# Performance work log

Measured on AMD Instinct MI355X. Metric: run time of the kernel, lower is better.

The kernel has to match this reference:

```python
import jax, jax.numpy as jnp
import numpy as np

B, N, D, H = 2, 2048, 1024, 16
HD = D // H
EPS = 1e-5

def _ln(x, g, b):
    m = jnp.mean(x, axis=-1, keepdims=True)
    v = jnp.mean((x - m) ** 2, axis=-1, keepdims=True)
    return (x - m) * jax.lax.rsqrt(v + EPS) * g + b

def setup_inputs() -> dict:
    key = jax.random.key(0)
    ks = jax.random.split(key, 16)
    s = 0.02
    inp = {
        'x': jax.random.normal(ks[0], (B, N, D), jnp.float32),
        'ln1_g': jnp.ones((D,), jnp.float32), 'ln1_b': jnp.zeros((D,), jnp.float32),
        'w_in': jax.random.normal(ks[1], (D, D), jnp.float32) * s, 'b_in': jnp.zeros((D,), jnp.float32),
        'wq': jax.random.normal(ks[2], (D, D), jnp.float32) * s,
        'wk': jax.random.normal(ks[3], (D, D), jnp.float32) * s,
        'wv': jax.random.normal(ks[4], (D, D), jnp.float32) * s,
        'wo': jax.random.normal(ks[5], (D, D), jnp.float32) * s, 'bo': jnp.zeros((D,), jnp.float32),
        'ln2_g': jnp.ones((D,), jnp.float32), 'ln2_b': jnp.zeros((D,), jnp.float32),
        'w_up': jax.random.normal(ks[6], (D, 4 * D), jnp.float32) * s, 'b_up': jnp.zeros((4 * D,), jnp.float32),
        'w_gate': jax.random.normal(ks[7], (D, 4 * D), jnp.float32) * s, 'b_gate': jnp.zeros((4 * D,), jnp.float32),
        'w_down': jax.random.normal(ks[8], (4 * D, D), jnp.float32) * s, 'b_down': jnp.zeros((D,), jnp.float32),
        'top_k': 64,
    }
    return inp

def _sparse_attention(h, wq, wk, wv, wo, bo, top_k):
    q = (h @ wq).reshape(B, N, H, HD).transpose(0, 2, 1, 3)  # [B,H,N,hd]
    k = (h @ wk).reshape(B, N, H, HD).transpose(0, 2, 1, 3)
    v = (h @ wv).reshape(B, N, H, HD).transpose(0, 2, 1, 3)
    scale = HD ** -0.5
    scores = jnp.einsum('bhqd,bhkd->bhqk', q, k) * scale  # [B,H,N,N]
    if top_k < N:
        # keep top_k per row: threshold at the k-th largest score
        kth = jax.lax.top_k(scores, top_k)[0][..., -1:]
        scores = jnp.where(scores >= kth, scores, -jnp.inf)
    attn = jax.nn.softmax(scores, axis=-1)
    out = jnp.einsum('bhqk,bhkd->bhqd', attn, v)
    out = out.transpose(0, 2, 1, 3).reshape(B, N, D)
    return out @ wo + bo

def reference(x, ln1_g, ln1_b, w_in, b_in, wq, wk, wv, wo, bo,
              ln2_g, ln2_b, w_up, b_up, w_gate, b_gate, w_down, b_down, top_k):
    h = _ln(x, ln1_g, ln1_b) @ w_in + b_in
    h = h + _sparse_attention(h, wq, wk, wv, wo, bo, top_k)
    ff_in = _ln(h, ln2_g, ln2_b)
    gate = jax.nn.silu(ff_in @ w_gate + b_gate)
    ff = (ff_in @ w_up + b_up) * gate
    ff = ff @ w_down + b_down
    return h + ff
```

## Files before the change

kernel.cpp:

```cpp
#include <hip/hip_runtime.h>
#include <cstdint>


#define DEV __device__ __forceinline__

constexpr int B_  = 2;
constexpr int N_  = 2048;
constexpr int D_  = 1024;
constexpr int H_  = 16;
constexpr int HD_ = 64;
constexpr int M_  = B_ * N_;
constexpr float EPS_ = 1e-5f;

using short8 = __attribute__((ext_vector_type(8))) short;
using f32x4  = __attribute__((ext_vector_type(4))) float;

DEV float4 ld4(const float* p) { return *reinterpret_cast<const float4*>(p); }
DEV void   st4(float* p, float4 v) { *reinterpret_cast<float4*>(p) = v; }

DEV unsigned short bf16r(float x) {
  unsigned u = __float_as_uint(x);
  u += 0x7fffu + ((u >> 16) & 1u);
  return (unsigned short)(u >> 16);
}
DEV float bf2f(unsigned short h) { return __uint_as_float(((unsigned)h) << 16); }

DEV unsigned fkey(float f) {
  unsigned u = __float_as_uint(f);
  return u ^ ((unsigned)((int)u >> 31) | 0x80000000u);
}
DEV float fval(unsigned k) {
  unsigned u = (k & 0x80000000u) ? (k ^ 0x80000000u) : ~k;
  return __uint_as_float(u);
}

__global__ __launch_bounds__(256) void wconv_kernel(const float* __restrict__ W,
                                                    unsigned short* __restrict__ Thi,
                                                    unsigned short* __restrict__ Tlo,
                                                    int K, int N) {
  __shared__ float t[32][33];
  const int k0 = blockIdx.y * 32, n0 = blockIdx.x * 32;
  const int tid = threadIdx.x;
  const int r = tid >> 3, c4 = (tid & 7) * 4;
  float4 v = ld4(W + (size_t)(k0 + r) * N + n0 + c4);
  t[r][c4 + 0] = v.x; t[r][c4 + 1] = v.y; t[r][c4 + 2] = v.z; t[r][c4 + 3] = v.w;
  __syncthreads();
  const int n = tid >> 3, kc = (tid & 7) * 4;
  ushort4 hv, lv;
  {
    float x0 = t[kc + 0][n], x1 = t[kc + 1][n], x2 = t[kc + 2][n], x3 = t[kc + 3][n];
    hv.x = bf16r(x0); lv.x = bf16r(x0 - bf2f(hv.x));
    hv.y = bf16r(x1); lv.y = bf16r(x1 - bf2f(hv.y));
    hv.z = bf16r(x2); lv.z = bf16r(x2 - bf2f(hv.z));
    hv.w = bf16r(x3); lv.w = bf16r(x3 - bf2f(hv.w));
  }
  *reinterpret_cast<ushort4*>(&Thi[(size_t)(n0 + n) * K + k0 + kc]) = hv;
  *reinterpret_cast<ushort4*>(&Tlo[(size_t)(n0 + n) * K + k0 + kc]) = lv;
}

__global__ __launch_bounds__(256) void ln_kernel(const float* __restrict__ in,
                                                 const float* __restrict__ g,
                                                 const float* __restrict__ b,
                                                 unsigned short* __restrict__ ohi,
                                                 unsigned short* __restrict__ olo) {
  const int row = blockIdx.x;
  const int t = threadIdx.x;
  float4 v = ld4(in + (size_t)row * D_ + t * 4);
  float s  = v.x + v.y + v.z + v.w;
  float ss = v.x * v.x + v.y * v.y + v.z * v.z + v.w * v.w;
  #pragma unroll
  for (int o = 32; o; o >>= 1) { s += __shfl_down(s, o); ss += __shfl_down(ss, o); }
  __shared__ float rs[4], rss[4];
  const int wid = t >> 6, lane = t & 63;
  if (lane == 0) { rs[wid] = s; rss[wid] = ss; }
  __syncthreads();
  s  = rs[0] + rs[1] + rs[2] + rs[3];
  ss = rss[0] + rss[1] + rss[2] + rss[3];
  const float mean = s * (1.f / D_);
  const float var  = ss * (1.f / D_) - mean * mean;
  const float rstd = rsqrtf(var + EPS_);
  float4 gv = ld4(g + t * 4);
  float4 bv = ld4(b + t * 4);
  float o0 = (v.x - mean) * rstd * gv.x + bv.x;
  float o1 = (v.y - mean) * rstd * gv.y + bv.y;
  float o2 = (v.z - mean) * rstd * gv.z + bv.z;
  float o3 = (v.w - mean) * rstd * gv.w + bv.w;
  ushort4 hv, lv;
  hv.x = bf16r(o0); lv.x = bf16r(o0 - bf2f(hv.x));
  hv.y = bf16r(o1); lv.y = bf16r(o1 - bf2f(hv.y));
  hv.z = bf16r(o2); lv.z = bf16r(o2 - bf2f(hv.z));
  hv.w = bf16r(o3); lv.w = bf16r(o3 - bf2f(hv.w));
  *reinterpret_cast<ushort4*>(&ohi[(size_t)row * D_ + t * 4]) = hv;
  *reinterpret_cast<ushort4*>(&olo[(size_t)row * D_ + t * 4]) = lv;
}

enum { GO_PAIR_BIAS = 0, GO_F32 = 1, GO_F32_BIAS_RESPAIR = 2,
       GO_F32_BIAS_RESF32 = 3, GO_F32_RES_NB = 4, GO_PAIR_NB = 5 };

template <int EPI>
__global__ __launch_bounds__(256) void gemm_sb(const unsigned short* __restrict__ Ah,
                                               const unsigned short* __restrict__ Al,
                                               const unsigned short* __restrict__ Bh,
                                               const unsigned short* __restrict__ Bl,
                                               const float* __restrict__ bias,
                                               const unsigned short* __restrict__ Rh,
                                               const unsigned short* __restrict__ Rl,
                                               const float* __restrict__ Rf,
                                               unsigned short* __restrict__ Ohi,
                                               unsigned short* __restrict__ Olo,
                                               float* __restrict__ Of,
                                               int M, int N, int K) {
  __shared__ unsigned short Ahs[128 * 40], Als[128 * 40];
  __shared__ unsigned short Bhs[64 * 40],  Bls[64 * 40];
  const int tid = threadIdx.x;
  const int m0 = blockIdx.y * 128, n0 = blockIdx.x * 64;
  const int lane = tid & 63, w = tid >> 6;
  const int wr = w >> 1, wc = w & 1;

  const int rA0 = tid >> 2, rA1 = 64 + (tid >> 2), chA = (tid & 3) * 8;
  const int rB = tid >> 2,  chB = (tid & 3) * 8;
  const size_t gA0 = (size_t)(m0 + rA0) * K + chA;
  const size_t gA1 = (size_t)(m0 + rA1) * K + chA;
  const size_t gB  = (size_t)(n0 + rB) * K + chB;
  const int lA0 = rA0 * 40 + chA, lA1 = rA1 * 40 + chA, lB = rB * 40 + chB;

  f32x4 acc[4][2];
  #pragma unroll
  for (int i = 0; i < 4; ++i)
    #pragma unroll
    for (int j = 0; j < 2; ++j) acc[i][j] = f32x4{0.f, 0.f, 0.f, 0.f};

  const int fr = lane & 15, fk = (lane >> 4) * 8;
  const int arow0 = (wr * 64 + fr) * 40 + fk;
  const int brow0 = (wc * 32 + fr) * 40 + fk;

  for (int k0 = 0; k0 < K; k0 += 32) {
    short8 a0h = *reinterpret_cast<const short8*>(&Ah[gA0 + k0]);
    short8 a1h = *reinterpret_cast<const short8*>(&Ah[gA1 + k0]);
    short8 a0l = *reinterpret_cast<const short8*>(&Al[gA0 + k0]);
    short8 a1l = *reinterpret_cast<const short8*>(&Al[gA1 + k0]);
    short8 bh  = *reinterpret_cast<const short8*>(&Bh[gB + k0]);
    short8 bl  = *reinterpret_cast<const short8*>(&Bl[gB + k0]);
    __syncthreads();
    *reinterpret_cast<short8*>(&Ahs[lA0]) = a0h;
    *reinterpret_cast<short8*>(&Ahs[lA1]) = a1h;
    *reinterpret_cast<short8*>(&Als[lA0]) = a0l;
    *reinterpret_cast<short8*>(&Als[lA1]) = a1l;
    *reinterpret_cast<short8*>(&Bhs[lB])  = bh;
    *reinterpret_cast<short8*>(&Bls[lB])  = bl;
    __syncthreads();

    short8 amh[4], aml[4], bnh[2], bnl[2];
    #pragma unroll
    for (int mf = 0; mf < 4; ++mf) {
      amh[mf] = *reinterpret_cast<const short8*>(&Ahs[arow0 + mf * 16 * 40]);
      aml[mf] = *reinterpret_cast<const short8*>(&Als[arow0 + mf * 16 * 40]);
    }
    #pragma unroll
    for (int nf = 0; nf < 2; ++nf) {
      bnh[nf] = *reinterpret_cast<const short8*>(&Bhs[brow0 + nf * 16 * 40]);
      bnl[nf] = *reinterpret_cast<const short8*>(&Bls[brow0 + nf * 16 * 40]);
    }
    #pragma unroll
    for (int mf = 0; mf < 4; ++mf)
      #pragma unroll
      for (int nf = 0; nf < 2; ++nf) {
        acc[mf][nf] = __builtin_amdgcn_mfma_f32_16x16x32_bf16(amh[mf], bnh[nf], acc[mf][nf], 0, 0, 0);
        acc[mf][nf] = __builtin_amdgcn_mfma_f32_16x16x32_bf16(amh[mf], bnl[nf], acc[mf][nf], 0, 0, 0);
        acc[mf][nf] = __builtin_amdgcn_mfma_f32_16x16x32_bf16(aml[mf], bnh[nf], acc[mf][nf], 0, 0, 0);
      }
  }

  const int er = (lane >> 4) * 4, ec = lane & 15;
  #pragma unroll
  for (int mf = 0; mf < 4; ++mf)
    #pragma unroll
    for (int nf = 0; nf < 2; ++nf)
      #pragma unroll
      for (int j = 0; j < 4; ++j) {
        const int m = m0 + wr * 64 + mf * 16 + er + j;
        const int n = n0 + wc * 32 + nf * 16 + ec;
        float v = acc[mf][nf][j];
        if constexpr (EPI == GO_PAIR_BIAS || EPI == GO_F32_BIAS_RESPAIR ||
                      EPI == GO_F32_BIAS_RESF32) v += bias[n];
        const size_t idx = (size_t)m * N + n;
        if constexpr (EPI == GO_PAIR_BIAS || EPI == GO_PAIR_NB) {
          unsigned short h = bf16r(v);
          Ohi[idx] = h; Olo[idx] = bf16r(v - bf2f(h));
        } else if constexpr (EPI == GO_F32) {
          Of[idx] = v;
        } else if constexpr (EPI == GO_F32_BIAS_RESPAIR) {
          Of[idx] = v + bf2f(Rh[idx]) + bf2f(Rl[idx]);
        } else {
          Of[idx] = v + Rf[idx];
        }
      }
}

__global__ __launch_bounds__(256) void gemm_gateup(const unsigned short* __restrict__ Ah,
                                                   const unsigned short* __restrict__ Al,
                                                   const unsigned short* __restrict__ Gh,
                                                   const unsigned short* __restrict__ Gl,
                                                   const unsigned short* __restrict__ Uh,
                                                   const unsigned short* __restrict__ Ul,
                                                   const float* __restrict__ bg,
                                                   const float* __restrict__ bu,
                                                   unsigned short* __restrict__ Ohi,
                                                   unsigned short* __restrict__ Olo,
                                                   int M, int N, int K) {
  __shared__ unsigned short Ahs[128 * 40], Als[128 * 40];
  __shared__ unsigned short Ghs[64 * 40], Gls[64 * 40], Uhs[64 * 40], Uls[64 * 40];
  const int tid = threadIdx.x;
  const int m0 = blockIdx.y * 128, n0 = blockIdx.x * 64;
  const int lane = tid & 63, w = tid >> 6;
  const int wr = w >> 1, wc = w & 1;

  const int rA0 = tid >> 2, rA1 = 64 + (tid >> 2), chA = (tid & 3) * 8;
  const int rB = tid >> 2, chB = (tid & 3) * 8;
  const size_t gA0 = (size_t)(m0 + rA0) * K + chA;
  const size_t gA1 = (size_t)(m0 + rA1) * K + chA;
  const size_t gB  = (size_t)(n0 + rB) * K + chB;
  const int lA0 = rA0 * 40 + chA, lA1 = rA1 * 40 + chA, lB = rB * 40 + chB;

  f32x4 accg[4][2], accu[4][2];
  #pragma unroll
  for (int i = 0; i < 4; ++i)
    #pragma unroll
    for (int j = 0; j < 2; ++j) {
      accg[i][j] = f32x4{0.f, 0.f, 0.f, 0.f};
      accu[i][j] = f32x4{0.f, 0.f, 0.f, 0.f};
    }

  const int fr = lane & 15, fk = (lane >> 4) * 8;
  const int arow0 = (wr * 64 + fr) * 40 + fk;
  const int brow0 = (wc * 32 + fr) * 40 + fk;

  for (int k0 = 0; k0 < K; k0 += 32) {
    short8 a0h = *reinterpret_cast<const short8*>(&Ah[gA0 + k0]);
    short8 a1h = *reinterpret_cast<const short8*>(&Ah[gA1 + k0]);
    short8 a0l = *reinterpret_cast<const short8*>(&Al[gA0 + k0]);
    short8 a1l = *reinterpret_cast<const short8*>(&Al[gA1 + k0]);
    short8 gh = *reinterpret_cast<const short8*>(&Gh[gB + k0]);
    short8 gl = *reinterpret_cast<const short8*>(&Gl[gB + k0]);
    short8 uh = *reinterpret_cast<const short8*>(&Uh[gB + k0]);
    short8 ul = *reinterpret_cast<const short8*>(&Ul[gB + k0]);
    __syncthreads();
    *reinterpret_cast<short8*>(&Ahs[lA0]) = a0h;
    *reinterpret_cast<short8*>(&Ahs[lA1]) = a1h;
    *reinterpret_cast<short8*>(&Als[lA0]) = a0l;
    *reinterpret_cast<short8*>(&Als[lA1]) = a1l;
    *reinterpret_cast<short8*>(&Ghs[lB]) = gh;
    *reinterpret_cast<short8*>(&Gls[lB]) = gl;
    *reinterpret_cast<short8*>(&Uhs[lB]) = uh;
    *reinterpret_cast<short8*>(&Uls[lB]) = ul;
    __syncthreads();

    short8 amh[4], aml[4];
    #pragma unroll
    for (int mf = 0; mf < 4; ++mf) {
      amh[mf] = *reinterpret_cast<const short8*>(&Ahs[arow0 + mf * 16 * 40]);
      aml[mf] = *reinterpret_cast<const short8*>(&Als[arow0 + mf * 16 * 40]);
    }
    #pragma unroll
    for (int nf = 0; nf < 2; ++nf) {
      short8 gnh = *reinterpret_cast<const short8*>(&Ghs[brow0 + nf * 16 * 40]);
      short8 gnl = *reinterpret_cast<const short8*>(&Gls[brow0 + nf * 16 * 40]);
      short8 unh = *reinterpret_cast<const short8*>(&Uhs[brow0 + nf * 16 * 40]);
      short8 unl = *reinterpret_cast<const short8*>(&Uls[brow0 + nf * 16 * 40]);
      #pragma unroll
      for (int mf = 0; mf < 4; ++mf) {
        accg[mf][nf] = __builtin_amdgcn_mfma_f32_16x16x32_bf16(amh[mf], gnh, accg[mf][nf], 0, 0, 0);
        accg[mf][nf] = __builtin_amdgcn_mfma_f32_16x16x32_bf16(amh[mf], gnl, accg[mf][nf], 0, 0, 0);
        accg[mf][nf] = __builtin_amdgcn_mfma_f32_16x16x32_bf16(aml[mf], gnh, accg[mf][nf], 0, 0, 0);
        accu[mf][nf] = __builtin_amdgcn_mfma_f32_16x16x32_bf16(amh[mf], unh, accu[mf][nf], 0, 0, 0);
        accu[mf][nf] = __builtin_amdgcn_mfma_f32_16x16x32_bf16(amh[mf], unl, accu[mf][nf], 0, 0, 0);
        accu[mf][nf] = __builtin_amdgcn_mfma_f32_16x16x32_bf16(aml[mf], unh, accu[mf][nf], 0, 0, 0);
      }
    }
  }

  const int er = (lane >> 4) * 4, ec = lane & 15;
  #pragma unroll
  for (int mf = 0; mf < 4; ++mf)
    #pragma unroll
    for (int nf = 0; nf < 2; ++nf)
      #pragma unroll
      for (int j = 0; j < 4; ++j) {
        const int m = m0 + wr * 64 + mf * 16 + er + j;
        const int n = n0 + wc * 32 + nf * 16 + ec;
        float g = accg[mf][nf][j] + bg[n];
        float u = accu[mf][nf][j] + bu[n];
        float f = (g / (1.f + expf(-g))) * u;
        const size_t idx = (size_t)m * N + n;
        unsigned short h = bf16r(f);
        Ohi[idx] = h; Olo[idx] = bf16r(f - bf2f(h));
      }
}

__global__ __launch_bounds__(256) void attn_kernel(
    const unsigned short* __restrict__ qh, const unsigned short* __restrict__ ql,
    const unsigned short* __restrict__ kh, const unsigned short* __restrict__ kl,
    const float* __restrict__ vm,
    unsigned short* __restrict__ aoh, unsigned short* __restrict__ aol,
    const int* __restrict__ topk_p) {
  constexpr int QB = 16;
  constexpr int NJ = N_ / 64;
  __shared__ float Sb[QB][513];
  __shared__ int   selIdx[4][128];
  __shared__ float selS[4][128];

  const int tid = threadIdx.x;
  const int lane = tid & 63, w = tid >> 6;
  const int bid = ((blockIdx.x & 7) << 9) | (blockIdx.x >> 3);
  const int qt = bid & 127;
  const int hh = (bid >> 7) & (H_ - 1);
  const int bb = bid >> 11;
  const int q0 = qt * QB;

  const int fr = lane & 15;
  const int fk = (lane >> 4) * 8;

  const size_t qbase = ((size_t)(bb * N_ + q0 + fr)) * D_ + hh * HD_ + fk;
  short8 ah0 = *reinterpret_cast<const short8*>(qh + qbase);
  short8 ah1 = *reinterpret_cast<const short8*>(qh + qbase + 32);
  short8 al0 = *reinterpret_cast<const short8*>(ql + qbase);
  short8 al1 = *reinterpret_cast<const short8*>(ql + qbase + 32);

  const int c0 = w * 512;
  const size_t kwb = ((size_t)(bb * N_ + c0 + fr)) * D_ + hh * HD_ + fk;

  f32x4 acc[32];
  #pragma unroll
  for (int ct = 0; ct < 32; ++ct) acc[ct] = f32x4{0.f, 0.f, 0.f, 0.f};

  #pragma unroll
  for (int ct = 0; ct < 32; ++ct) {
    const size_t kb0 = kwb + (size_t)ct * 16 * D_;
    short8 bh0 = *reinterpret_cast<const short8*>(kh + kb0);
    short8 bh1 = *reinterpret_cast<const short8*>(kh + kb0 + 32);
    short8 bl0 = *reinterpret_cast<const short8*>(kl + kb0);
    short8 bl1 = *reinterpret_cast<const short8*>(kl + kb0 + 32);
    acc[ct] = __builtin_amdgcn_mfma_f32_16x16x32_bf16(ah0, bh0, acc[ct], 0, 0, 0);
    acc[ct] = __builtin_amdgcn_mfma_f32_16x16x32_bf16(ah0, bl0, acc[ct], 0, 0, 0);
    acc[ct] = __builtin_amdgcn_mfma_f32_16x16x32_bf16(al0, bh0, acc[ct], 0, 0, 0);
    acc[ct] = __builtin_amdgcn_mfma_f32_16x16x32_bf16(ah1, bh1, acc[ct], 0, 0, 0);
    acc[ct] = __builtin_amdgcn_mfma_f32_16x16x32_bf16(ah1, bl1, acc[ct], 0, 0, 0);
    acc[ct] = __builtin_amdgcn_mfma_f32_16x16x32_bf16(al1, bh1, acc[ct], 0, 0, 0);
  }

  unsigned key[4][NJ];
  const int r0 = (lane >> 4) * 4;
  #pragma unroll
  for (int c = 0; c < 4; ++c) {
    if (w == c) {
      #pragma unroll
      for (int ct = 0; ct < 32; ++ct) {
        const int col = ct * 16 + fr;
        #pragma unroll
        for (int j = 0; j < 4; ++j)
          Sb[r0 + j][col] = acc[ct][j] * 0.125f;
      }
    }
    __syncthreads();
    #pragma unroll
    for (int rr = 0; rr < 4; ++rr) {
      const int row = w + rr * 4;
      #pragma unroll
      for (int jj = 0; jj < 8; ++jj)
        key[rr][c * 8 + jj] = fkey(Sb[row][jj * 64 + lane]);
    }
    __syncthreads();
  }

  int topk = *topk_p;
  if (topk > N_) topk = N_;
  const float* Vb = vm + (size_t)bb * N_ * D_ + hh * HD_;

  #pragma unroll
  for (int rr = 0; rr < 4; ++rr) {
    unsigned kmax = 0;
    #pragma unroll
    for (int j = 0; j < NJ; ++j) kmax = (key[rr][j] > kmax) ? key[rr][j] : kmax;
    #pragma unroll
    for (int o = 32; o; o >>= 1) {
      unsigned t = __shfl_xor(kmax, o);
      kmax = (t > kmax) ? t : kmax;
    }
    const float smax = fval(kmax);

    unsigned thr = 0u;
    if (topk < N_) {
      for (int bit = 31; bit >= 0; --bit) {
        const unsigned cand = thr | (1u << bit);
        int c = 0;
        #pragma unroll
        for (int j = 0; j < NJ; ++j)
          c += __popcll(__ballot(key[rr][j] >= cand));
        if (c >= topk) {
          thr = cand;
          if (c == topk) break;
        }
      }
    }

    int base = 0;
    #pragma unroll
    for (int j = 0; j < NJ; ++j) {
      const bool sel = key[rr][j] >= thr;
      const unsigned long long m = __ballot(sel);
      if (sel) {
        const int pos = base + (int)__popcll(m & ((1ull << lane) - 1ull));
        if (pos < 128) {
          selIdx[w][pos] = j * 64 + lane;
          selS[w][pos]   = fval(key[rr][j]);
        }
      }
      base += (int)__popcll(m);
    }
    const int cnt = (base > 128) ? 128 : base;

    float wsum = 0.f;
    if (lane < cnt) {
      float e = expf(selS[w][lane] - smax);
      selS[w][lane] = e; wsum += e;
    }
    if (lane + 64 < cnt) {
      float e = expf(selS[w][lane + 64] - smax);
      selS[w][lane + 64] = e; wsum += e;
    }
    #pragma unroll
    for (int o = 32; o; o >>= 1) wsum += __shfl_xor(wsum, o);

    float outv = 0.f;
    int i = 0;
    for (; i + 16 <= cnt; i += 16) {
      int ix[16]; float wv[16], vv[16];
      #pragma unroll
      for (int t = 0; t < 16; ++t) {
        ix[t] = selIdx[w][i + t];
        wv[t] = selS[w][i + t];
      }
      #pragma unroll
      for (int t = 0; t < 16; ++t) vv[t] = Vb[(size_t)ix[t] * D_ + lane];
      #pragma unroll
      for (int t = 0; t < 16; ++t) outv += wv[t] * vv[t];
    }
    for (; i < cnt; ++i)
      outv += selS[w][i] * Vb[(size_t)selIdx[w][i] * D_ + lane];

    const float o = outv / wsum;
    const size_t oidx = ((size_t)bb * N_ + q0 + w + rr * 4) * D_ + hh * HD_ + lane;
    unsigned short hsh = bf16r(o);
    aoh[oidx] = hsh; aol[oidx] = bf16r(o - bf2f(hsh));
  }
}

extern "C" void kernel_launch(void* const* d_in, const int* in_sizes, int n_in,
                              void* d_out, int out_size, void* d_ws, size_t ws_size,
                              hipStream_t stream) {
  const float* x      = (const float*)d_in[0];
  const float* ln1_g  = (const float*)d_in[1];
  const float* ln1_b  = (const float*)d_in[2];
  const float* w_in   = (const float*)d_in[3];
  const float* b_in   = (const float*)d_in[4];
  const float* wq     = (const float*)d_in[5];
  const float* wk     = (const float*)d_in[6];
  const float* wv     = (const float*)d_in[7];
  const float* wo     = (const float*)d_in[8];
  const float* bo     = (const float*)d_in[9];
  const float* ln2_g  = (const float*)d_in[10];
  const float* ln2_b  = (const float*)d_in[11];
  const float* w_up   = (const float*)d_in[12];
  const float* b_up   = (const float*)d_in[13];
  const float* w_gate = (const float*)d_in[14];
  const float* b_gate = (const float*)d_in[15];
  const float* w_down = (const float*)d_in[16];
  const float* b_down = (const float*)d_in[17];
  const int*   topk   = (const int*)d_in[18];
  float* out = (float*)d_out;

  char* p = (char*)d_ws;
  const size_t MB = 1024 * 1024;
  unsigned short* Wi_h = (unsigned short*)(p + 0 * MB);
  unsigned short* Wi_l = (unsigned short*)(p + 2 * MB);
  unsigned short* Wq_h = (unsigned short*)(p + 4 * MB);
  unsigned short* Wq_l = (unsigned short*)(p + 6 * MB);
  unsigned short* Wk_h = (unsigned short*)(p + 8 * MB);
  unsigned short* Wk_l = (unsigned short*)(p + 10 * MB);
  unsigned short* Wv_h = (unsigned short*)(p + 12 * MB);
  unsigned short* Wv_l = (unsigned short*)(p + 14 * MB);
  unsigned short* Wo_h = (unsigned short*)(p + 16 * MB);
  unsigned short* Wo_l = (unsigned short*)(p + 18 * MB);
  unsigned short* Wd0_h = (unsigned short*)(p + 20 * MB);
  unsigned short* Wd0_l = (unsigned short*)(p + 24 * MB);
  unsigned short* Wd1_h = (unsigned short*)(p + 28 * MB);
  unsigned short* Wd1_l = (unsigned short*)(p + 32 * MB);
  unsigned short* hp_h = (unsigned short*)(p + 36 * MB);
  unsigned short* hp_l = (unsigned short*)(p + 44 * MB);
  unsigned short* ff_h = (unsigned short*)(p + 36 * MB);
  unsigned short* ff_l = (unsigned short*)(p + 44 * MB);
  unsigned short* xn_h = (unsigned short*)(p + 52 * MB);
  unsigned short* xn_l = (unsigned short*)(p + 60 * MB);
  unsigned short* q_h  = (unsigned short*)(p + 52 * MB);
  unsigned short* q_l  = (unsigned short*)(p + 60 * MB);
  unsigned short* k_h  = (unsigned short*)(p + 68 * MB);
  unsigned short* k_l  = (unsigned short*)(p + 76 * MB);
  float*          vb   = (float*)(p + 84 * MB);
  unsigned short* Wg_h = (unsigned short*)(p + 52 * MB);
  unsigned short* Wg_l = (unsigned short*)(p + 60 * MB);
  unsigned short* Wu_h = (unsigned short*)(p + 68 * MB);
  unsigned short* Wu_l = (unsigned short*)(p + 76 * MB);
  unsigned short* f1_h = (unsigned short*)(p + 84 * MB);
  unsigned short* ao_h = (unsigned short*)(p + 0 * MB);
  unsigned short* ao_l = (unsigned short*)(p + 8 * MB);
  unsigned short* f1_l = (unsigned short*)(p + 0 * MB);

  const dim3 blk(256);
  const dim3 gW1k(32, 32);
  const dim3 gWgu(128, 32);
  const dim3 gWd(32, 64);
  const dim3 g1024(16, 32);
  const dim3 g2048(32, 32);

  wconv_kernel<<<gW1k, blk, 0, stream>>>(w_in, Wi_h, Wi_l, 1024, 1024);
  wconv_kernel<<<gW1k, blk, 0, stream>>>(wq, Wq_h, Wq_l, 1024, 1024);
  wconv_kernel<<<gW1k, blk, 0, stream>>>(wk, Wk_h, Wk_l, 1024, 1024);
  wconv_kernel<<<gW1k, blk, 0, stream>>>(wv, Wv_h, Wv_l, 1024, 1024);
  wconv_kernel<<<gW1k, blk, 0, stream>>>(wo, Wo_h, Wo_l, 1024, 1024);
  wconv_kernel<<<gWd, blk, 0, stream>>>(w_down,               Wd0_h, Wd0_l, 2048, 1024);
  wconv_kernel<<<gWd, blk, 0, stream>>>(w_down + 2048 * 1024, Wd1_h, Wd1_l, 2048, 1024);

  ln_kernel<<<M_, blk, 0, stream>>>(x, ln1_g, ln1_b, xn_h, xn_l);
  gemm_sb<GO_PAIR_BIAS><<<g1024, blk, 0, stream>>>(xn_h, xn_l, Wi_h, Wi_l, b_in,
      nullptr, nullptr, nullptr, hp_h, hp_l, nullptr, M_, 1024, 1024);
  gemm_sb<GO_PAIR_NB><<<g1024, blk, 0, stream>>>(hp_h, hp_l, Wq_h, Wq_l, nullptr,
      nullptr, nullptr, nullptr, q_h, q_l, nullptr, M_, 1024, 1024);
  gemm_sb<GO_PAIR_NB><<<g1024, blk, 0, stream>>>(hp_h, hp_l, Wk_h, Wk_l, nullptr,
      nullptr, nullptr, nullptr, k_h, k_l, nullptr, M_, 1024, 1024);
  gemm_sb<GO_F32><<<g1024, blk, 0, stream>>>(hp_h, hp_l, Wv_h, Wv_l, nullptr,
      nullptr, nullptr, nullptr, nullptr, nullptr, vb, M_, 1024, 1024);

  attn_kernel<<<B_ * H_ * (N_ / 16), blk, 0, stream>>>(q_h, q_l, k_h, k_l, vb,
      ao_h, ao_l, topk);

  wconv_kernel<<<gWgu, blk, 0, stream>>>(w_gate, Wg_h, Wg_l, 1024, 4096);
  wconv_kernel<<<gWgu, blk, 0, stream>>>(w_up,   Wu_h, Wu_l, 1024, 4096);

  gemm_sb<GO_F32_BIAS_RESPAIR><<<g1024, blk, 0, stream>>>(ao_h, ao_l, Wo_h, Wo_l, bo,
      hp_h, hp_l, nullptr, nullptr, nullptr, out, M_, 1024, 1024);

  ln_kernel<<<M_, blk, 0, stream>>>(out, ln2_g, ln2_b, ff_h, ff_l);

  gemm_gateup<<<g2048, blk, 0, stream>>>(ff_h, ff_l,
      Wg_h, Wg_l, Wu_h, Wu_l, b_gate, b_up, f1_h, f1_l, M_, 2048, 1024);
  gemm_sb<GO_F32_BIAS_RESF32><<<g1024, blk, 0, stream>>>(f1_h, f1_l, Wd0_h, Wd0_l,
      b_down, nullptr, nullptr, out, nullptr, nullptr, out, M_, 1024, 2048);
  gemm_gateup<<<g2048, blk, 0, stream>>>(ff_h, ff_l,
      Wg_h + (size_t)2048 * 1024, Wg_l + (size_t)2048 * 1024,
      Wu_h + (size_t)2048 * 1024, Wu_l + (size_t)2048 * 1024,
      b_gate + 2048, b_up + 2048, f1_h, f1_l, M_, 2048, 1024);
  gemm_sb<GO_F32_RES_NB><<<g1024, blk, 0, stream>>>(f1_h, f1_l, Wd1_h, Wd1_l,
      nullptr, nullptr, nullptr, out, nullptr, nullptr, out, M_, 1024, 2048);
}
```

Baseline: 1.333 ms.

## Chunk QK^T score computation across waves to cut accumulator registers in attention

Restructures the attention score computation so each of the four column chunks is computed cooperatively by all waves (128 columns each), holding 8 accumulator tiles instead of 32 per wave. This lowers VGPR pressure, and the launch bounds now request 2 blocks per CU to raise occupancy. Every wave now writes its part of the score buffer in each chunk instead of only one wave writing at a time, which removes the serialized write phases. Barrier placement changes, and the key array still holds 128 registers, so the compiler may spill to meet the occupancy target.

```diff
diff --git a/kernel.cpp b/kernel.cpp
--- a/kernel.cpp
+++ b/kernel.cpp
@@ -297,7 +297,7 @@
       }
 }
 
-__global__ __launch_bounds__(256) void attn_kernel(
+__global__ __launch_bounds__(256, 2) void attn_kernel(
     const unsigned short* __restrict__ qh, const unsigned short* __restrict__ ql,
     const unsigned short* __restrict__ kh, const unsigned short* __restrict__ kl,
     const float* __restrict__ vm,
@@ -326,50 +326,48 @@
   short8 al0 = *reinterpret_cast<const short8*>(ql + qbase);
   short8 al1 = *reinterpret_cast<const short8*>(ql + qbase + 32);
 
-  const int c0 = w * 512;
-  const size_t kwb = ((size_t)(bb * N_ + c0 + fr)) * D_ + hh * HD_ + fk;
-
-  f32x4 acc[32];
-  #pragma unroll
-  for (int ct = 0; ct < 32; ++ct) acc[ct] = f32x4{0.f, 0.f, 0.f, 0.f};
-
-  #pragma unroll
-  for (int ct = 0; ct < 32; ++ct) {
-    const size_t kb0 = kwb + (size_t)ct * 16 * D_;
-    short8 bh0 = *reinterpret_cast<const short8*>(kh + kb0);
-    short8 bh1 = *reinterpret_cast<const short8*>(kh + kb0 + 32);
-    short8 bl0 = *reinterpret_cast<const short8*>(kl + kb0);
-    short8 bl1 = *reinterpret_cast<const short8*>(kl + kb0 + 32);
-    acc[ct] = __builtin_amdgcn_mfma_f32_16x16x32_bf16(ah0, bh0, acc[ct], 0, 0, 0);
-    acc[ct] = __builtin_amdgcn_mfma_f32_16x16x32_bf16(ah0, bl0, acc[ct], 0, 0, 0);
-    acc[ct] = __builtin_amdgcn_mfma_f32_16x16x32_bf16(al0, bh0, acc[ct], 0, 0, 0);
-    acc[ct] = __builtin_amdgcn_mfma_f32_16x16x32_bf16(ah1, bh1, acc[ct], 0, 0, 0);
-    acc[ct] = __builtin_amdgcn_mfma_f32_16x16x32_bf16(ah1, bl1, acc[ct], 0, 0, 0);
-    acc[ct] = __builtin_amdgcn_mfma_f32_16x16x32_bf16(al1, bh1, acc[ct], 0, 0, 0);
-  }
-
   unsigned key[4][NJ];
   const int r0 = (lane >> 4) * 4;
-  #pragma unroll
-  for (int c = 0; c < 4; ++c) {
-    if (w == c) {
-      #pragma unroll
-      for (int ct = 0; ct < 32; ++ct) {
-        const int col = ct * 16 + fr;
-        #pragma unroll
-        for (int j = 0; j < 4; ++j)
-          Sb[r0 + j][col] = acc[ct][j] * 0.125f;
-      }
-    }
+
+  for (int cc = 0; cc < 4; ++cc) {
+    const int colbase = cc * 512 + w * 128;
+    const size_t kwb = ((size_t)(bb * N_ + colbase + fr)) * D_ + hh * HD_ + fk;
+
+    f32x4 acc[8];
+    #pragma unroll
+    for (int ctl = 0; ctl < 8; ++ctl) acc[ctl] = f32x4{0.f, 0.f, 0.f, 0.f};
+    #pragma unroll
+    for (int ctl = 0; ctl < 8; ++ctl) {
+      const size_t kb0 = kwb + (size_t)ctl * 16 * D_;
+      short8 bh0 = *reinterpret_cast<const short8*>(kh + kb0);
+      short8 bh1 = *reinterpret_cast<const short8*>(kh + kb0 + 32);
+      short8 bl0 = *reinterpret_cast<const short8*>(kl + kb0);
+      short8 bl1 = *reinterpret_cast<const short8*>(kl + kb0 + 32);
+      acc[ctl] = __builtin_amdgcn_mfma_f32_16x16x32_bf16(ah0, bh0, acc[ctl], 0, 0, 0);
+      acc[ctl] = __builtin_amdgcn_mfma_f32_16x16x32_bf16(ah0, bl0, acc[ctl], 0, 0, 0);
+      acc[ctl] = __builtin_amdgcn_mfma_f32_16x16x32_bf16(al0, bh0, acc[ctl], 0, 0, 0);
+      acc[ctl] = __builtin_amdgcn_mfma_f32_16x16x32_bf16(ah1, bh1, acc[ctl], 0, 0, 0);
+      acc[ctl] = __builtin_amdgcn_mfma_f32_16x16x32_bf16(ah1, bl1, acc[ctl], 0, 0, 0);
+      acc[ctl] = __builtin_amdgcn_mfma_f32_16x16x32_bf16(al1, bh1, acc[ctl], 0, 0, 0);
+    }
+
     __syncthreads();
+    #pragma unroll
+    for (int ctl = 0; ctl < 8; ++ctl) {
+      const int col = w * 128 + ctl * 16 + fr;
+      #pragma unroll
+      for (int j = 0; j < 4; ++j)
+        Sb[r0 + j][col] = acc[ctl][j] * 0.125f;
+    }
+    __syncthreads();
+
     #pragma unroll
     for (int rr = 0; rr < 4; ++rr) {
       const int row = w + rr * 4;
       #pragma unroll
       for (int jj = 0; jj < 8; ++jj)
-        key[rr][c * 8 + jj] = fkey(Sb[row][jj * 64 + lane]);
-    }
-    __syncthreads();
+        key[rr][cc * 8 + jj] = fkey(Sb[row][jj * 64 + lane]);
+    }
   }
 
   int topk = *topk_p;
```

New measurement: 1.313 ms. About the same (-1.6%).
